# Performance work log

Measured on AMD Instinct MI355X. Metric: run time of the kernel, lower is better.

The kernel has to match this reference:

```python
import jax, jax.numpy as jnp
import numpy as np

N_DST = (50000, 25000, 12500)


def setup_inputs() -> dict:
    key = jax.random.key(0)
    ks = jax.random.split(key, 20)
    d_in, d_h, d_out = 256, 256, 128
    n_src = 100000
    inp = {}
    inp["x"] = jax.random.normal(ks[0], (n_src, d_in), dtype=jnp.float32)
    s = lambda k, sh, fan: jax.random.normal(k, sh, dtype=jnp.float32) / np.sqrt(fan)
    inp["Wn0"] = s(ks[1], (d_in, d_h), d_in)
    inp["Ws0"] = s(ks[2], (d_in, d_h), d_in)
    inp["b0"] = jnp.zeros((d_h,), jnp.float32)
    inp["Wn1"] = s(ks[3], (d_h, d_h), d_h)
    inp["Ws1"] = s(ks[4], (d_h, d_h), d_h)
    inp["b1"] = jnp.zeros((d_h,), jnp.float32)
    inp["Wn2"] = s(ks[5], (d_h, d_out), d_h)
    inp["Ws2"] = s(ks[6], (d_h, d_out), d_h)
    inp["b2"] = jnp.zeros((d_out,), jnp.float32)
    inp["src0"] = jax.random.randint(ks[7], (500000,), 0, n_src, dtype=jnp.int32)
    inp["dst0"] = jax.random.randint(ks[8], (500000,), 0, N_DST[0], dtype=jnp.int32)
    inp["src1"] = jax.random.randint(ks[9], (250000,), 0, N_DST[0], dtype=jnp.int32)
    inp["dst1"] = jax.random.randint(ks[10], (250000,), 0, N_DST[1], dtype=jnp.int32)
    inp["src2"] = jax.random.randint(ks[11], (125000,), 0, N_DST[1], dtype=jnp.int32)
    inp["dst2"] = jax.random.randint(ks[12], (125000,), 0, N_DST[2], dtype=jnp.int32)
    return inp


def _sage_conv(h_src, src, dst, n_dst, Wn, Ws, b):
    # mean aggregation over incoming neighbors, then linear + self linear
    msg = h_src[src]                                   # [E, d] gather
    agg = jax.ops.segment_sum(msg, dst, num_segments=n_dst)
    cnt = jax.ops.segment_sum(jnp.ones((src.shape[0], 1), h_src.dtype), dst,
                              num_segments=n_dst)
    mean = agg / jnp.maximum(cnt, 1.0)
    return mean @ Wn + h_src[:n_dst] @ Ws + b


def reference(x, Wn0, Ws0, b0, Wn1, Ws1, b1, Wn2, Ws2, b2,
              src0, dst0, src1, dst1, src2, dst2):
    h = _sage_conv(x, src0, dst0, N_DST[0], Wn0, Ws0, b0)
    h = jax.nn.relu(h)
    h = _sage_conv(h, src1, dst1, N_DST[1], Wn1, Ws1, b1)
    h = jax.nn.relu(h)
    h = _sage_conv(h, src2, dst2, N_DST[2], Wn2, Ws2, b2)
    return h
```

## Files before the change

kernel.cpp:

```cpp
#include <hip/hip_runtime.h>
#include <hip/hip_bf16.h>


typedef __attribute__((ext_vector_type(8))) short bf16x8;
typedef __attribute__((ext_vector_type(4))) float floatx4;

constexpr int M0 = 50000, M1 = 25000, M2 = 12500;
constexpr int NODE_OFF1 = 50000, NODE_OFF2 = 75000, M_TOT = 87500;
constexpr int NSRC = 100000;
constexpr int NPART = 8;
constexpr int CAP = 64;

__device__ inline unsigned short f2bf(float f) {
    union { float f; unsigned int u; } v{f};
    unsigned int u = v.u;
    return (unsigned short)((u + 0x7FFFu + ((u >> 16) & 1u)) >> 16);
}
__device__ inline float bf2f(unsigned short h) {
    union { unsigned int u; float f; } v{(unsigned int)h << 16};
    return v.f;
}

constexpr int CAST_B = 25000;
constexpr int PREP_B = 640;

__global__ __launch_bounds__(256) void front_kernel(
    const float* __restrict__ x, unsigned short* __restrict__ xb,
    const float* __restrict__ Wn0, const float* __restrict__ Ws0,
    const float* __restrict__ Wn1, const float* __restrict__ Ws1,
    const float* __restrict__ Wn2, const float* __restrict__ Ws2,
    unsigned short* __restrict__ Wt0, unsigned short* __restrict__ Wt1,
    unsigned short* __restrict__ Wt2,
    const int* __restrict__ src0, const int* __restrict__ dst0,
    const int* __restrict__ src1, const int* __restrict__ dst1,
    const int* __restrict__ src2, const int* __restrict__ dst2,
    int* __restrict__ wptr, int* __restrict__ bkt,
    int E0, int E1, int E2)
{
    const int blk = blockIdx.x;
    if (blk < CAST_B) {
        long i = (long)blk * 256 + threadIdx.x;
        float4 v = reinterpret_cast<const float4*>(x)[i];
        ushort4 o{f2bf(v.x), f2bf(v.y), f2bf(v.z), f2bf(v.w)};
        reinterpret_cast<ushort4*>(xb)[i] = o;
    } else if (blk < CAST_B + PREP_B) {
        int b = blk - CAST_B;
        const float* Wn; const float* Ws; unsigned short* Wt; int N; int base;
        if (b < 256)      { Wn = Wn0; Ws = Ws0; Wt = Wt0; N = 256; base = 0; }
        else if (b < 512) { Wn = Wn1; Ws = Ws1; Wt = Wt1; N = 256; base = 256; }
        else              { Wn = Wn2; Ws = Ws2; Wt = Wt2; N = 128; base = 512; }
        int idx = (b - base) * 256 + threadIdx.x;
        int n = idx >> 8, k = idx & 255;
        if (n >= N) return;
        Wt[(size_t)n * 512 + k]       = f2bf(Wn[(size_t)k * N + n]);
        Wt[(size_t)n * 512 + 256 + k] = f2bf(Ws[(size_t)k * N + n]);
    } else {
        const int b = blk - CAST_B - PREP_B;
        const int part = b & (NPART - 1);
        const int i = (b >> 3) * 256 + threadIdx.x;
        const int lo = (int)(((long)M_TOT * part) / NPART);
        const int hi = (int)(((long)M_TOT * (part + 1)) / NPART);
        int node, s;
        if (i < E0) {
            node = dst0[i]; s = src0[i];
        } else if (i < E0 + E1) {
            int j = i - E0; node = NODE_OFF1 + dst1[j]; s = src1[j];
        } else if (i < E0 + E1 + E2) {
            int j = i - E0 - E1; node = NODE_OFF2 + dst2[j]; s = src2[j];
        } else return;
        if (node >= lo && node < hi) {
            int p = atomicAdd(&wptr[node], 1);
            if (p < CAP) bkt[(size_t)node * CAP + p] = s;
        }
    }
}


__global__ __launch_bounds__(256) void aggregate_mean_bf16(
    const unsigned short* __restrict__ h, const int* __restrict__ wptr,
    const int* __restrict__ bkt, unsigned short* __restrict__ mean, int M)
{
    int gid = blockIdx.x * 256 + threadIdx.x;
    int node = gid >> 6;
    int lane = gid & 63;
    if (node >= M) return;
    int cnt = min(wptr[node], CAP);
    const int* lst = bkt + (size_t)node * CAP;
    float ax = 0.f, ay = 0.f, az = 0.f, aw = 0.f;
    int e = 0;
    for (; e + 8 <= cnt; e += 8) {
        int sidx = lst[e + (lane & 7)];
#pragma unroll
        for (int j = 0; j < 8; ++j) {
            int s = __shfl(sidx, j);
            ushort4 v = *(const ushort4*)(h + (size_t)s * 256 + lane * 4);
            ax += bf2f(v.x); ay += bf2f(v.y); az += bf2f(v.z); aw += bf2f(v.w);
        }
    }
    for (; e < cnt; ++e) {
        int s = lst[e];
        ushort4 v = *(const ushort4*)(h + (size_t)s * 256 + lane * 4);
        ax += bf2f(v.x); ay += bf2f(v.y); az += bf2f(v.z); aw += bf2f(v.w);
    }
    float invd = 1.0f / (float)max(cnt, 1);
    ushort4 o{f2bf(ax * invd), f2bf(ay * invd), f2bf(az * invd), f2bf(aw * invd)};
    *(ushort4*)(mean + (size_t)node * 256 + lane * 4) = o;
}


template <int RELU, int OUT_BF16>
__global__ __launch_bounds__(256) void sage_mfma(
    const unsigned short* __restrict__ A1,
    const unsigned short* __restrict__ A2,
    const unsigned short* __restrict__ Wt,
    const float* __restrict__ bias,
    void* __restrict__ out, int M, int N)
{
    constexpr int PK = 64 + 8;
    __shared__ unsigned short sA[128][PK];
    __shared__ unsigned short sB[128][PK];

    const int tid = threadIdx.x;
    const int bm = blockIdx.y * 128;
    const int bn = blockIdx.x * 128;
    const int wid = tid >> 6, lane = tid & 63;
    const int wm = (wid >> 1) * 64;
    const int wn = (wid & 1) * 64;
    const int quad = lane >> 4, l16 = lane & 15;

    const int sr = tid >> 1;
    const int sc = (tid & 1) * 32;

    floatx4 acc[4][4] = {};

    for (int k0 = 0; k0 < 512; k0 += 64) {
        const unsigned short* Ab = (k0 < 256) ? A1 : A2;
        const int ak = k0 & 255;
        const float4* ag = (const float4*)(Ab + (size_t)(bm + sr) * 256 + ak + sc);
        float4 a0 = ag[0], a1 = ag[1], a2 = ag[2], a3 = ag[3];
        const float4* bg = (const float4*)(Wt + (size_t)(bn + sr) * 512 + k0 + sc);
        float4 b0 = bg[0], b1 = bg[1], b2 = bg[2], b3 = bg[3];
        __syncthreads();
        *(float4*)&sA[sr][sc]      = a0;
        *(float4*)&sA[sr][sc + 8]  = a1;
        *(float4*)&sA[sr][sc + 16] = a2;
        *(float4*)&sA[sr][sc + 24] = a3;
        *(float4*)&sB[sr][sc]      = b0;
        *(float4*)&sB[sr][sc + 8]  = b1;
        *(float4*)&sB[sr][sc + 16] = b2;
        *(float4*)&sB[sr][sc + 24] = b3;
        __syncthreads();
#pragma unroll
        for (int ks = 0; ks < 64; ks += 32) {
            bf16x8 af[4], bfr[4];
#pragma unroll
            for (int i = 0; i < 4; ++i)
                af[i] = *(const bf16x8*)&sA[wm + i * 16 + l16][ks + quad * 8];
#pragma unroll
            for (int j = 0; j < 4; ++j)
                bfr[j] = *(const bf16x8*)&sB[wn + j * 16 + l16][ks + quad * 8];
#pragma unroll
            for (int i = 0; i < 4; ++i)
#pragma unroll
                for (int j = 0; j < 4; ++j)
                    acc[i][j] = __builtin_amdgcn_mfma_f32_16x16x32_bf16(
                        af[i], bfr[j], acc[i][j], 0, 0, 0);
        }
    }

#pragma unroll
    for (int j = 0; j < 4; ++j) {
        int col = bn + wn + j * 16 + l16;
        float bcol = bias[col];
#pragma unroll
        for (int i = 0; i < 4; ++i) {
#pragma unroll
            for (int r = 0; r < 4; ++r) {
                int row = bm + wm + i * 16 + quad * 4 + r;
                if (row < M) {
                    float v = acc[i][j][r] + bcol;
                    if (RELU) v = fmaxf(v, 0.0f);
                    if (OUT_BF16)
                        ((unsigned short*)out)[(size_t)row * N + col] = f2bf(v);
                    else
                        ((float*)out)[(size_t)row * N + col] = v;
                }
            }
        }
    }
}


extern "C" void kernel_launch(void* const* d_in, const int* in_sizes, int n_in,
                              void* d_out, int out_size, void* d_ws, size_t ws_size,
                              hipStream_t stream)
{
    const float* x   = (const float*)d_in[0];
    const float* Wn0 = (const float*)d_in[1];
    const float* Ws0 = (const float*)d_in[2];
    const float* b0  = (const float*)d_in[3];
    const float* Wn1 = (const float*)d_in[4];
    const float* Ws1 = (const float*)d_in[5];
    const float* b1  = (const float*)d_in[6];
    const float* Wn2 = (const float*)d_in[7];
    const float* Ws2 = (const float*)d_in[8];
    const float* b2  = (const float*)d_in[9];
    const int* src0 = (const int*)d_in[10];
    const int* dst0 = (const int*)d_in[11];
    const int* src1 = (const int*)d_in[12];
    const int* dst1 = (const int*)d_in[13];
    const int* src2 = (const int*)d_in[14];
    const int* dst2 = (const int*)d_in[15];
    const int E0 = in_sizes[10], E1 = in_sizes[12], E2 = in_sizes[14];
    const int E_tot = E0 + E1 + E2;

    unsigned short* xb   = (unsigned short*)d_ws;
    unsigned short* mean = xb   + (size_t)NSRC  * 256;
    unsigned short* h0   = mean + (size_t)50048 * 256;
    unsigned short* h1   = h0   + (size_t)50048 * 256;
    unsigned short* Wt0  = h1   + (size_t)25088 * 256;
    unsigned short* Wt1  = Wt0  + 256 * 512;
    unsigned short* Wt2  = Wt1  + 256 * 512;
    int* wptr   = (int*)(Wt2 + 128 * 512);
    int* bkt    = wptr + M_TOT;
    float* outp = (float*)d_out;

    hipMemsetAsync(wptr, 0, (size_t)M_TOT * sizeof(int), stream);

    const int sc_b = (E_tot + 255) / 256;
    front_kernel<<<dim3(CAST_B + PREP_B + NPART * sc_b), dim3(256), 0, stream>>>(
        x, xb, Wn0, Ws0, Wn1, Ws1, Wn2, Ws2, Wt0, Wt1, Wt2,
        src0, dst0, src1, dst1, src2, dst2, wptr, bkt, E0, E1, E2);

    auto run_layer = [&](const unsigned short* hin, int node_off, int M,
                         const unsigned short* Wt, const float* b,
                         void* hout, int N, bool relu, bool out_bf16) {
        aggregate_mean_bf16<<<dim3((M * 64 + 255) / 256), dim3(256), 0, stream>>>(
            hin, wptr + node_off, bkt + (size_t)node_off * CAP, mean, M);
        dim3 g(N / 128, (M + 127) / 128);
        if (out_bf16)
            sage_mfma<1, 1><<<g, dim3(256), 0, stream>>>(mean, hin, Wt, b, hout, M, N);
        else
            sage_mfma<0, 0><<<g, dim3(256), 0, stream>>>(mean, hin, Wt, b, hout, M, N);
    };

    run_layer(xb, 0,         M0, Wt0, b0, h0,   256, true,  true);
    run_layer(h0, NODE_OFF1, M1, Wt1, b1, h1,   256, true,  true);
    run_layer(h1, NODE_OFF2, M2, Wt2, b2, outp, 128, false, false);
}
```

Before: 392.8 us.

## Interleave cast and scatter blocks; aggregate two nodes per wavefront

The front kernel now interleaves its x-cast blocks with the edge-scatter blocks, so bandwidth-bound casting overlaps with atomic-heavy bucketing instead of running in separate phases, and the weight-prep blocks move to the end. The aggregation kernel now has each wavefront process two destination nodes at once: it loads the whole neighbor list with one coalesced read per node and issues the two nodes' gathers in the same loop, giving more memory-level parallelism. This risks divergence when the two nodes' degrees differ and halves the number of launched waves.

New measurement: 409.1 us. 4.1% more time.

```diff
diff --git a/kernel.cpp b/kernel.cpp
--- a/kernel.cpp
+++ b/kernel.cpp
@@ -35,29 +35,32 @@
     const int* __restrict__ src1, const int* __restrict__ dst1,
     const int* __restrict__ src2, const int* __restrict__ dst2,
     int* __restrict__ wptr, int* __restrict__ bkt,
-    int E0, int E1, int E2)
-{
-    const int blk = blockIdx.x;
-    if (blk < CAST_B) {
-        long i = (long)blk * 256 + threadIdx.x;
+    int E0, int E1, int E2, int SC_B)
+{
+    const int b = blockIdx.x;
+    const int minb = (CAST_B < SC_B) ? CAST_B : SC_B;
+    const int inter = 2 * minb;
+    int role, idx;
+    if (b < inter) {
+        role = b & 1;
+        idx = b >> 1;
+    } else {
+        int r = b - inter;
+        int scatRem = SC_B - minb;
+        int castRem = CAST_B - minb;
+        if (r < scatRem)                { role = 1; idx = minb + r; }
+        else if (r < scatRem + castRem) { role = 0; idx = minb + (r - scatRem); }
+        else                            { role = 2; idx = r - scatRem - castRem; }
+    }
+
+    if (role == 0) {
+        long i = (long)idx * 256 + threadIdx.x;
         float4 v = reinterpret_cast<const float4*>(x)[i];
         ushort4 o{f2bf(v.x), f2bf(v.y), f2bf(v.z), f2bf(v.w)};
         reinterpret_cast<ushort4*>(xb)[i] = o;
-    } else if (blk < CAST_B + PREP_B) {
-        int b = blk - CAST_B;
-        const float* Wn; const float* Ws; unsigned short* Wt; int N; int base;
-        if (b < 256)      { Wn = Wn0; Ws = Ws0; Wt = Wt0; N = 256; base = 0; }
-        else if (b < 512) { Wn = Wn1; Ws = Ws1; Wt = Wt1; N = 256; base = 256; }
-        else              { Wn = Wn2; Ws = Ws2; Wt = Wt2; N = 128; base = 512; }
-        int idx = (b - base) * 256 + threadIdx.x;
-        int n = idx >> 8, k = idx & 255;
-        if (n >= N) return;
-        Wt[(size_t)n * 512 + k]       = f2bf(Wn[(size_t)k * N + n]);
-        Wt[(size_t)n * 512 + 256 + k] = f2bf(Ws[(size_t)k * N + n]);
-    } else {
-        const int b = blk - CAST_B - PREP_B;
-        const int part = b & (NPART - 1);
-        const int i = (b >> 3) * 256 + threadIdx.x;
+    } else if (role == 1) {
+        const int part = idx & (NPART - 1);
+        const int i = (idx >> 3) * 256 + threadIdx.x;
         const int lo = (int)(((long)M_TOT * part) / NPART);
         const int hi = (int)(((long)M_TOT * (part + 1)) / NPART);
         int node, s;
@@ -72,6 +75,17 @@
             int p = atomicAdd(&wptr[node], 1);
             if (p < CAP) bkt[(size_t)node * CAP + p] = s;
         }
+    } else {
+        int bb = idx;
+        const float* Wn; const float* Ws; unsigned short* Wt; int N; int base;
+        if (bb < 256)      { Wn = Wn0; Ws = Ws0; Wt = Wt0; N = 256; base = 0; }
+        else if (bb < 512) { Wn = Wn1; Ws = Ws1; Wt = Wt1; N = 256; base = 256; }
+        else               { Wn = Wn2; Ws = Ws2; Wt = Wt2; N = 128; base = 512; }
+        int idx2 = (bb - base) * 256 + threadIdx.x;
+        int n = idx2 >> 8, k = idx2 & 255;
+        if (n >= N) return;
+        Wt[(size_t)n * 512 + k]       = f2bf(Wn[(size_t)k * N + n]);
+        Wt[(size_t)n * 512 + 256 + k] = f2bf(Ws[(size_t)k * N + n]);
     }
 }
 
@@ -81,30 +95,39 @@
     const int* __restrict__ bkt, unsigned short* __restrict__ mean, int M)
 {
     int gid = blockIdx.x * 256 + threadIdx.x;
-    int node = gid >> 6;
+    int w = gid >> 6;
     int lane = gid & 63;
-    if (node >= M) return;
-    int cnt = min(wptr[node], CAP);
-    const int* lst = bkt + (size_t)node * CAP;
-    float ax = 0.f, ay = 0.f, az = 0.f, aw = 0.f;
-    int e = 0;
-    for (; e + 8 <= cnt; e += 8) {
-        int sidx = lst[e + (lane & 7)];
-#pragma unroll
-        for (int j = 0; j < 8; ++j) {
-            int s = __shfl(sidx, j);
+    int half = (M + 1) >> 1;
+    if (w >= half) return;
+    int n0 = w, n1 = w + half;
+    bool has1 = (n1 < M);
+    int c0 = min(wptr[n0], CAP);
+    int c1 = has1 ? min(wptr[n1], CAP) : 0;
+    int sidx0 = bkt[(size_t)n0 * CAP + lane];
+    int sidx1 = has1 ? bkt[(size_t)n1 * CAP + lane] : 0;
+    float a0x = 0.f, a0y = 0.f, a0z = 0.f, a0w = 0.f;
+    float a1x = 0.f, a1y = 0.f, a1z = 0.f, a1w = 0.f;
+    int mx = max(c0, c1);
+    for (int j = 0; j < mx; ++j) {
+        if (j < c0) {
+            int s = __shfl(sidx0, j);
             ushort4 v = *(const ushort4*)(h + (size_t)s * 256 + lane * 4);
-            ax += bf2f(v.x); ay += bf2f(v.y); az += bf2f(v.z); aw += bf2f(v.w);
-        }
-    }
-    for (; e < cnt; ++e) {
-        int s = lst[e];
-        ushort4 v = *(const ushort4*)(h + (size_t)s * 256 + lane * 4);
-        ax += bf2f(v.x); ay += bf2f(v.y); az += bf2f(v.z); aw += bf2f(v.w);
-    }
-    float invd = 1.0f / (float)max(cnt, 1);
-    ushort4 o{f2bf(ax * invd), f2bf(ay * invd), f2bf(az * invd), f2bf(aw * invd)};
-    *(ushort4*)(mean + (size_t)node * 256 + lane * 4) = o;
+            a0x += bf2f(v.x); a0y += bf2f(v.y); a0z += bf2f(v.z); a0w += bf2f(v.w);
+        }
+        if (j < c1) {
+            int s = __shfl(sidx1, j);
+            ushort4 v = *(const ushort4*)(h + (size_t)s * 256 + lane * 4);
+            a1x += bf2f(v.x); a1y += bf2f(v.y); a1z += bf2f(v.z); a1w += bf2f(v.w);
+        }
+    }
+    float i0 = 1.0f / (float)max(c0, 1);
+    ushort4 o0{f2bf(a0x * i0), f2bf(a0y * i0), f2bf(a0z * i0), f2bf(a0w * i0)};
+    *(ushort4*)(mean + (size_t)n0 * 256 + lane * 4) = o0;
+    if (has1) {
+        float i1 = 1.0f / (float)max(c1, 1);
+        ushort4 o1{f2bf(a1x * i1), f2bf(a1y * i1), f2bf(a1z * i1), f2bf(a1w * i1)};
+        *(ushort4*)(mean + (size_t)n1 * 256 + lane * 4) = o1;
+    }
 }
 
 
@@ -228,14 +251,16 @@
     hipMemsetAsync(wptr, 0, (size_t)M_TOT * sizeof(int), stream);
 
     const int sc_b = (E_tot + 255) / 256;
-    front_kernel<<<dim3(CAST_B + PREP_B + NPART * sc_b), dim3(256), 0, stream>>>(
+    const int SC_B = NPART * sc_b;
+    front_kernel<<<dim3(CAST_B + PREP_B + SC_B), dim3(256), 0, stream>>>(
         x, xb, Wn0, Ws0, Wn1, Ws1, Wn2, Ws2, Wt0, Wt1, Wt2,
-        src0, dst0, src1, dst1, src2, dst2, wptr, bkt, E0, E1, E2);
+        src0, dst0, src1, dst1, src2, dst2, wptr, bkt, E0, E1, E2, SC_B);
 
     auto run_layer = [&](const unsigned short* hin, int node_off, int M,
                          const unsigned short* Wt, const float* b,
                          void* hout, int N, bool relu, bool out_bf16) {
-        aggregate_mean_bf16<<<dim3((M * 64 + 255) / 256), dim3(256), 0, stream>>>(
+        int halfw = (M + 1) >> 1;
+        aggregate_mean_bf16<<<dim3((halfw * 64 + 255) / 256), dim3(256), 0, stream>>>(
             hin, wptr + node_off, bkt + (size_t)node_off * CAP, mean, M);
         dim3 g(N / 128, (M + 127) / 128);
         if (out_bf16)
```

## Fuse all stages into one persistent cooperative kernel with grid syncs

Applied to the files above, without the earlier changes.

Replaces the memset plus seven separate launches with a single cooperative persistent kernel that loops over work units in grid-stride fashion and separates stages with grid.sync. The aim is to remove launch overhead and inter-kernel gaps. The aggregation now loads the whole bucket list with one coalesced read and picks indices with shuffles. The risk is that persistent blocks, capped at three per CU by launch bounds, underfill the wide cast and gather stages. Shared memory from the GEMM also limits occupancy in the memory-bound phases.

Measured after the change: 1.041 ms. 165% more time.

```diff
diff --git a/kernel.cpp b/kernel.cpp
--- a/kernel.cpp
+++ b/kernel.cpp
@@ -1,5 +1,8 @@
 #include <hip/hip_runtime.h>
 #include <hip/hip_bf16.h>
+#include <hip/hip_cooperative_groups.h>
+
+namespace cg = cooperative_groups;
 
 
 typedef __attribute__((ext_vector_type(8))) short bf16x8;
@@ -10,6 +13,20 @@
 constexpr int NSRC = 100000;
 constexpr int NPART = 8;
 constexpr int CAP = 64;
+constexpr int PK = 72;
+constexpr int CAST_B = 25000;
+constexpr int PREP_B = 640;
+
+struct SageArgs {
+    const float* x;
+    const float *Wn0, *Ws0, *Wn1, *Ws1, *Wn2, *Ws2;
+    const float *b0, *b1, *b2;
+    const int *src0, *dst0, *src1, *dst1, *src2, *dst2;
+    int E0, E1, E2, SC_B;
+    unsigned short *xb, *mean, *h0, *h1, *Wt0, *Wt1, *Wt2;
+    int *wptr, *bkt;
+    float* out;
+};
 
 __device__ inline unsigned short f2bf(float f) {
     union { float f; unsigned int u; } v{f};
@@ -21,173 +38,215 @@
     return v.f;
 }
 
-constexpr int CAST_B = 25000;
-constexpr int PREP_B = 640;
-
-__global__ __launch_bounds__(256) void front_kernel(
-    const float* __restrict__ x, unsigned short* __restrict__ xb,
-    const float* __restrict__ Wn0, const float* __restrict__ Ws0,
-    const float* __restrict__ Wn1, const float* __restrict__ Ws1,
-    const float* __restrict__ Wn2, const float* __restrict__ Ws2,
-    unsigned short* __restrict__ Wt0, unsigned short* __restrict__ Wt1,
-    unsigned short* __restrict__ Wt2,
-    const int* __restrict__ src0, const int* __restrict__ dst0,
-    const int* __restrict__ src1, const int* __restrict__ dst1,
-    const int* __restrict__ src2, const int* __restrict__ dst2,
-    int* __restrict__ wptr, int* __restrict__ bkt,
-    int E0, int E1, int E2)
-{
-    const int blk = blockIdx.x;
-    if (blk < CAST_B) {
-        long i = (long)blk * 256 + threadIdx.x;
-        float4 v = reinterpret_cast<const float4*>(x)[i];
-        ushort4 o{f2bf(v.x), f2bf(v.y), f2bf(v.z), f2bf(v.w)};
-        reinterpret_cast<ushort4*>(xb)[i] = o;
-    } else if (blk < CAST_B + PREP_B) {
-        int b = blk - CAST_B;
-        const float* Wn; const float* Ws; unsigned short* Wt; int N; int base;
-        if (b < 256)      { Wn = Wn0; Ws = Ws0; Wt = Wt0; N = 256; base = 0; }
-        else if (b < 512) { Wn = Wn1; Ws = Ws1; Wt = Wt1; N = 256; base = 256; }
-        else              { Wn = Wn2; Ws = Ws2; Wt = Wt2; N = 128; base = 512; }
-        int idx = (b - base) * 256 + threadIdx.x;
-        int n = idx >> 8, k = idx & 255;
-        if (n >= N) return;
-        Wt[(size_t)n * 512 + k]       = f2bf(Wn[(size_t)k * N + n]);
-        Wt[(size_t)n * 512 + 256 + k] = f2bf(Ws[(size_t)k * N + n]);
-    } else {
-        const int b = blk - CAST_B - PREP_B;
-        const int part = b & (NPART - 1);
-        const int i = (b >> 3) * 256 + threadIdx.x;
-        const int lo = (int)(((long)M_TOT * part) / NPART);
-        const int hi = (int)(((long)M_TOT * (part + 1)) / NPART);
-        int node, s;
-        if (i < E0) {
-            node = dst0[i]; s = src0[i];
-        } else if (i < E0 + E1) {
-            int j = i - E0; node = NODE_OFF1 + dst1[j]; s = src1[j];
-        } else if (i < E0 + E1 + E2) {
-            int j = i - E0 - E1; node = NODE_OFF2 + dst2[j]; s = src2[j];
-        } else return;
-        if (node >= lo && node < hi) {
-            int p = atomicAdd(&wptr[node], 1);
-            if (p < CAP) bkt[(size_t)node * CAP + p] = s;
+__device__ __forceinline__ void stage_zero(const SageArgs& a, int nb)
+{
+    for (int i = blockIdx.x * 256 + threadIdx.x; i < M_TOT; i += nb * 256)
+        a.wptr[i] = 0;
+}
+
+__device__ __forceinline__ void stage_front(const SageArgs& a, int nb)
+{
+    const int E0 = a.E0, E1 = a.E1, E2 = a.E2;
+    const int units = CAST_B + PREP_B + a.SC_B;
+    for (int u = blockIdx.x; u < units; u += nb) {
+        if (u < CAST_B) {
+            long i = (long)u * 256 + threadIdx.x;
+            float4 v = reinterpret_cast<const float4*>(a.x)[i];
+            ushort4 o{f2bf(v.x), f2bf(v.y), f2bf(v.z), f2bf(v.w)};
+            reinterpret_cast<ushort4*>(a.xb)[i] = o;
+        } else if (u < CAST_B + PREP_B) {
+            int b = u - CAST_B;
+            const float* Wn; const float* Ws; unsigned short* Wt; int N; int base;
+            if (b < 256)      { Wn = a.Wn0; Ws = a.Ws0; Wt = a.Wt0; N = 256; base = 0; }
+            else if (b < 512) { Wn = a.Wn1; Ws = a.Ws1; Wt = a.Wt1; N = 256; base = 256; }
+            else              { Wn = a.Wn2; Ws = a.Ws2; Wt = a.Wt2; N = 128; base = 512; }
+            int idx = (b - base) * 256 + threadIdx.x;
+            int n = idx >> 8, k = idx & 255;
+            if (n < N) {
+                Wt[(size_t)n * 512 + k]       = f2bf(Wn[(size_t)k * N + n]);
+                Wt[(size_t)n * 512 + 256 + k] = f2bf(Ws[(size_t)k * N + n]);
+            }
+        } else {
+            const int b = u - CAST_B - PREP_B;
+            const int part = b & (NPART - 1);
+            const int i = (b >> 3) * 256 + threadIdx.x;
+            const int lo = (int)(((long)M_TOT * part) / NPART);
+            const int hi = (int)(((long)M_TOT * (part + 1)) / NPART);
+            int node = -1, s = 0;
+            if (i < E0) {
+                node = a.dst0[i]; s = a.src0[i];
+            } else if (i < E0 + E1) {
+                int j = i - E0; node = NODE_OFF1 + a.dst1[j]; s = a.src1[j];
+            } else if (i < E0 + E1 + E2) {
+                int j = i - E0 - E1; node = NODE_OFF2 + a.dst2[j]; s = a.src2[j];
+            }
+            if (node >= lo && node < hi) {
+                int p = atomicAdd(&a.wptr[node], 1);
+                if (p < CAP) a.bkt[(size_t)node * CAP + p] = s;
+            }
         }
     }
 }
 
-
-__global__ __launch_bounds__(256) void aggregate_mean_bf16(
-    const unsigned short* __restrict__ h, const int* __restrict__ wptr,
-    const int* __restrict__ bkt, unsigned short* __restrict__ mean, int M)
-{
-    int gid = blockIdx.x * 256 + threadIdx.x;
-    int node = gid >> 6;
-    int lane = gid & 63;
-    if (node >= M) return;
-    int cnt = min(wptr[node], CAP);
-    const int* lst = bkt + (size_t)node * CAP;
-    float ax = 0.f, ay = 0.f, az = 0.f, aw = 0.f;
-    int e = 0;
-    for (; e + 8 <= cnt; e += 8) {
-        int sidx = lst[e + (lane & 7)];
-#pragma unroll
-        for (int j = 0; j < 8; ++j) {
-            int s = __shfl(sidx, j);
+__device__ __forceinline__ void stage_agg(
+    const unsigned short* __restrict__ h, const int* __restrict__ wp,
+    const int* __restrict__ bk, unsigned short* __restrict__ mean,
+    int M, int nb)
+{
+    const int lane = threadIdx.x & 63;
+    const int wid = threadIdx.x >> 6;
+    for (int node = blockIdx.x * 4 + wid; node < M; node += nb * 4) {
+        int cnt = min(wp[node], CAP);
+        int sidx = bk[(size_t)node * CAP + lane];
+        float ax = 0.f, ay = 0.f, az = 0.f, aw = 0.f;
+        int e = 0;
+        for (; e + 8 <= cnt; e += 8) {
+#pragma unroll
+            for (int j = 0; j < 8; ++j) {
+                int s = __shfl(sidx, e + j);
+                ushort4 v = *(const ushort4*)(h + (size_t)s * 256 + lane * 4);
+                ax += bf2f(v.x); ay += bf2f(v.y); az += bf2f(v.z); aw += bf2f(v.w);
+            }
+        }
+        for (; e < cnt; ++e) {
+            int s = __shfl(sidx, e);
             ushort4 v = *(const ushort4*)(h + (size_t)s * 256 + lane * 4);
             ax += bf2f(v.x); ay += bf2f(v.y); az += bf2f(v.z); aw += bf2f(v.w);
         }
+        float invd = 1.0f / (float)max(cnt, 1);
+        ushort4 o{f2bf(ax * invd), f2bf(ay * invd), f2bf(az * invd), f2bf(aw * invd)};
+        *(ushort4*)(mean + (size_t)node * 256 + lane * 4) = o;
     }
-    for (; e < cnt; ++e) {
-        int s = lst[e];
-        ushort4 v = *(const ushort4*)(h + (size_t)s * 256 + lane * 4);
-        ax += bf2f(v.x); ay += bf2f(v.y); az += bf2f(v.z); aw += bf2f(v.w);
-    }
-    float invd = 1.0f / (float)max(cnt, 1);
-    ushort4 o{f2bf(ax * invd), f2bf(ay * invd), f2bf(az * invd), f2bf(aw * invd)};
-    *(ushort4*)(mean + (size_t)node * 256 + lane * 4) = o;
-}
-
+}
 
 template <int RELU, int OUT_BF16>
-__global__ __launch_bounds__(256) void sage_mfma(
-    const unsigned short* __restrict__ A1,
-    const unsigned short* __restrict__ A2,
-    const unsigned short* __restrict__ Wt,
-    const float* __restrict__ bias,
-    void* __restrict__ out, int M, int N)
-{
-    constexpr int PK = 64 + 8;
-    __shared__ unsigned short sA[128][PK];
-    __shared__ unsigned short sB[128][PK];
-
+__device__ __forceinline__ void stage_gemm(
+    unsigned short (*sA)[PK], unsigned short (*sB)[PK],
+    const unsigned short* __restrict__ A1, const unsigned short* __restrict__ A2,
+    const unsigned short* __restrict__ Wt, const float* __restrict__ bias,
+    void* __restrict__ out, int M, int N, int nb)
+{
     const int tid = threadIdx.x;
-    const int bm = blockIdx.y * 128;
-    const int bn = blockIdx.x * 128;
+    const int tiles_m = (M + 127) >> 7;
+    const int tiles_n = N >> 7;
+    const int tiles = tiles_m * tiles_n;
     const int wid = tid >> 6, lane = tid & 63;
     const int wm = (wid >> 1) * 64;
     const int wn = (wid & 1) * 64;
     const int quad = lane >> 4, l16 = lane & 15;
-
     const int sr = tid >> 1;
     const int sc = (tid & 1) * 32;
 
-    floatx4 acc[4][4] = {};
-
-    for (int k0 = 0; k0 < 512; k0 += 64) {
-        const unsigned short* Ab = (k0 < 256) ? A1 : A2;
-        const int ak = k0 & 255;
-        const float4* ag = (const float4*)(Ab + (size_t)(bm + sr) * 256 + ak + sc);
-        float4 a0 = ag[0], a1 = ag[1], a2 = ag[2], a3 = ag[3];
-        const float4* bg = (const float4*)(Wt + (size_t)(bn + sr) * 512 + k0 + sc);
-        float4 b0 = bg[0], b1 = bg[1], b2 = bg[2], b3 = bg[3];
-        __syncthreads();
-        *(float4*)&sA[sr][sc]      = a0;
-        *(float4*)&sA[sr][sc + 8]  = a1;
-        *(float4*)&sA[sr][sc + 16] = a2;
-        *(float4*)&sA[sr][sc + 24] = a3;
-        *(float4*)&sB[sr][sc]      = b0;
-        *(float4*)&sB[sr][sc + 8]  = b1;
-        *(float4*)&sB[sr][sc + 16] = b2;
-        *(float4*)&sB[sr][sc + 24] = b3;
-        __syncthreads();
-#pragma unroll
-        for (int ks = 0; ks < 64; ks += 32) {
-            bf16x8 af[4], bfr[4];
-#pragma unroll
-            for (int i = 0; i < 4; ++i)
-                af[i] = *(const bf16x8*)&sA[wm + i * 16 + l16][ks + quad * 8];
-#pragma unroll
-            for (int j = 0; j < 4; ++j)
-                bfr[j] = *(const bf16x8*)&sB[wn + j * 16 + l16][ks + quad * 8];
-#pragma unroll
-            for (int i = 0; i < 4; ++i)
+    for (int t = blockIdx.x; t < tiles; t += nb) {
+        const int bm = (t / tiles_n) * 128;
+        const int bn = (t % tiles_n) * 128;
+        floatx4 acc[4][4] = {};
+
+        for (int k0 = 0; k0 < 512; k0 += 64) {
+            const unsigned short* Ab = (k0 < 256) ? A1 : A2;
+            const int ak = k0 & 255;
+            const float4* ag = (const float4*)(Ab + (size_t)(bm + sr) * 256 + ak + sc);
+            float4 a0 = ag[0], a1 = ag[1], a2 = ag[2], a3 = ag[3];
+            const float4* bg = (const float4*)(Wt + (size_t)(bn + sr) * 512 + k0 + sc);
+            float4 b0 = bg[0], b1 = bg[1], b2 = bg[2], b3 = bg[3];
+            __syncthreads();
+            *(float4*)&sA[sr][sc]      = a0;
+            *(float4*)&sA[sr][sc + 8]  = a1;
+            *(float4*)&sA[sr][sc + 16] = a2;
+            *(float4*)&sA[sr][sc + 24] = a3;
+            *(float4*)&sB[sr][sc]      = b0;
+            *(float4*)&sB[sr][sc + 8]  = b1;
+            *(float4*)&sB[sr][sc + 16] = b2;
+            *(float4*)&sB[sr][sc + 24] = b3;
+            __syncthreads();
+#pragma unroll
+            for (int ks = 0; ks < 64; ks += 32) {
+                bf16x8 af[4], bfr[4];
+#pragma unroll
+                for (int i = 0; i < 4; ++i)
+                    af[i] = *(const bf16x8*)&sA[wm + i * 16 + l16][ks + quad * 8];
 #pragma unroll
                 for (int j = 0; j < 4; ++j)
-                    acc[i][j] = __builtin_amdgcn_mfma_f32_16x16x32_bf16(
-                        af[i], bfr[j], acc[i][j], 0, 0, 0);
+                    bfr[j] = *(const bf16x8*)&sB[wn + j * 16 + l16][ks + quad * 8];
+#pragma unroll
+                for (int i = 0; i < 4; ++i)
+#pragma unroll
+                    for (int j = 0; j < 4; ++j)
+                        acc[i][j] = __builtin_amdgcn_mfma_f32_16x16x32_bf16(
+                            af[i], bfr[j], acc[i][j], 0, 0, 0);
+            }
+        }
+
+#pragma unroll
+        for (int j = 0; j < 4; ++j) {
+            int col = bn + wn + j * 16 + l16;
+            float bcol = bias[col];
+#pragma unroll
+            for (int i = 0; i < 4; ++i) {
+#pragma unroll
+                for (int r = 0; r < 4; ++r) {
+                    int row = bm + wm + i * 16 + quad * 4 + r;
+                    if (row < M) {
+                        float v = acc[i][j][r] + bcol;
+                        if (RELU) v = fmaxf(v, 0.0f);
+                        if (OUT_BF16)
+                            ((unsigned short*)out)[(size_t)row * N + col] = f2bf(v);
+                        else
+                            ((float*)out)[(size_t)row * N + col] = v;
+                    }
+                }
+            }
         }
     }
-
-#pragma unroll
-    for (int j = 0; j < 4; ++j) {
-        int col = bn + wn + j * 16 + l16;
-        float bcol = bias[col];
-#pragma unroll
-        for (int i = 0; i < 4; ++i) {
-#pragma unroll
-            for (int r = 0; r < 4; ++r) {
-                int row = bm + wm + i * 16 + quad * 4 + r;
-                if (row < M) {
-                    float v = acc[i][j][r] + bcol;
-                    if (RELU) v = fmaxf(v, 0.0f);
-                    if (OUT_BF16)
-                        ((unsigned short*)out)[(size_t)row * N + col] = f2bf(v);
-                    else
-                        ((float*)out)[(size_t)row * N + col] = v;
-                }
-            }
-        }
-    }
+}
+
+
+__global__ __launch_bounds__(256, 3) void sage_all(SageArgs a)
+{
+    __shared__ unsigned short sA[128][PK];
+    __shared__ unsigned short sB[128][PK];
+    cg::grid_group grid = cg::this_grid();
+    const int nb = gridDim.x;
+
+    stage_zero(a, nb);
+    __threadfence(); grid.sync();
+
+    stage_front(a, nb);
+    __threadfence(); grid.sync();
+
+    stage_agg(a.xb, a.wptr, a.bkt, a.mean, M0, nb);
+    __threadfence(); grid.sync();
+    stage_gemm<1, 1>(sA, sB, a.mean, a.xb, a.Wt0, a.b0, a.h0, M0, 256, nb);
+    __threadfence(); grid.sync();
+
+    stage_agg(a.h0, a.wptr + NODE_OFF1, a.bkt + (size_t)NODE_OFF1 * CAP, a.mean, M1, nb);
+    __threadfence(); grid.sync();
+    stage_gemm<1, 1>(sA, sB, a.mean, a.h0, a.Wt1, a.b1, a.h1, M1, 256, nb);
+    __threadfence(); grid.sync();
+
+    stage_agg(a.h1, a.wptr + NODE_OFF2, a.bkt + (size_t)NODE_OFF2 * CAP, a.mean, M2, nb);
+    __threadfence(); grid.sync();
+    stage_gemm<0, 0>(sA, sB, a.mean, a.h1, a.Wt2, a.b2, a.out, M2, 128, nb);
+}
+
+
+__global__ __launch_bounds__(256) void k_zero(SageArgs a) { stage_zero(a, gridDim.x); }
+__global__ __launch_bounds__(256) void k_front(SageArgs a) { stage_front(a, gridDim.x); }
+__global__ __launch_bounds__(256) void k_agg(SageArgs a, int layer)
+{
+    if (layer == 0)      stage_agg(a.xb, a.wptr, a.bkt, a.mean, M0, gridDim.x);
+    else if (layer == 1) stage_agg(a.h0, a.wptr + NODE_OFF1,
+                                   a.bkt + (size_t)NODE_OFF1 * CAP, a.mean, M1, gridDim.x);
+    else                 stage_agg(a.h1, a.wptr + NODE_OFF2,
+                                   a.bkt + (size_t)NODE_OFF2 * CAP, a.mean, M2, gridDim.x);
+}
+__global__ __launch_bounds__(256) void k_gemm(SageArgs a, int layer)
+{
+    __shared__ unsigned short sA[128][PK];
+    __shared__ unsigned short sB[128][PK];
+    if (layer == 0)      stage_gemm<1, 1>(sA, sB, a.mean, a.xb, a.Wt0, a.b0, a.h0, M0, 256, gridDim.x);
+    else if (layer == 1) stage_gemm<1, 1>(sA, sB, a.mean, a.h0, a.Wt1, a.b1, a.h1, M1, 256, gridDim.x);
+    else                 stage_gemm<0, 0>(sA, sB, a.mean, a.h1, a.Wt2, a.b2, a.out, M2, 128, gridDim.x);
 }
 
 
@@ -195,56 +254,51 @@
                               void* d_out, int out_size, void* d_ws, size_t ws_size,
                               hipStream_t stream)
 {
-    const float* x   = (const float*)d_in[0];
-    const float* Wn0 = (const float*)d_in[1];
-    const float* Ws0 = (const float*)d_in[2];
-    const float* b0  = (const float*)d_in[3];
-    const float* Wn1 = (const float*)d_in[4];
-    const float* Ws1 = (const float*)d_in[5];
-    const float* b1  = (const float*)d_in[6];
-    const float* Wn2 = (const float*)d_in[7];
-    const float* Ws2 = (const float*)d_in[8];
-    const float* b2  = (const float*)d_in[9];
-    const int* src0 = (const int*)d_in[10];
-    const int* dst0 = (const int*)d_in[11];
-    const int* src1 = (const int*)d_in[12];
-    const int* dst1 = (const int*)d_in[13];
-    const int* src2 = (const int*)d_in[14];
-    const int* dst2 = (const int*)d_in[15];
-    const int E0 = in_sizes[10], E1 = in_sizes[12], E2 = in_sizes[14];
-    const int E_tot = E0 + E1 + E2;
-
-    unsigned short* xb   = (unsigned short*)d_ws;
-    unsigned short* mean = xb   + (size_t)NSRC  * 256;
-    unsigned short* h0   = mean + (size_t)50048 * 256;
-    unsigned short* h1   = h0   + (size_t)50048 * 256;
-    unsigned short* Wt0  = h1   + (size_t)25088 * 256;
-    unsigned short* Wt1  = Wt0  + 256 * 512;
-    unsigned short* Wt2  = Wt1  + 256 * 512;
-    int* wptr   = (int*)(Wt2 + 128 * 512);
-    int* bkt    = wptr + M_TOT;
-    float* outp = (float*)d_out;
-
-    hipMemsetAsync(wptr, 0, (size_t)M_TOT * sizeof(int), stream);
-
-    const int sc_b = (E_tot + 255) / 256;
-    front_kernel<<<dim3(CAST_B + PREP_B + NPART * sc_b), dim3(256), 0, stream>>>(
-        x, xb, Wn0, Ws0, Wn1, Ws1, Wn2, Ws2, Wt0, Wt1, Wt2,
-        src0, dst0, src1, dst1, src2, dst2, wptr, bkt, E0, E1, E2);
-
-    auto run_layer = [&](const unsigned short* hin, int node_off, int M,
-                         const unsigned short* Wt, const float* b,
-                         void* hout, int N, bool relu, bool out_bf16) {
-        aggregate_mean_bf16<<<dim3((M * 64 + 255) / 256), dim3(256), 0, stream>>>(
-            hin, wptr + node_off, bkt + (size_t)node_off * CAP, mean, M);
-        dim3 g(N / 128, (M + 127) / 128);
-        if (out_bf16)
-            sage_mfma<1, 1><<<g, dim3(256), 0, stream>>>(mean, hin, Wt, b, hout, M, N);
-        else
-            sage_mfma<0, 0><<<g, dim3(256), 0, stream>>>(mean, hin, Wt, b, hout, M, N);
-    };
-
-    run_layer(xb, 0,         M0, Wt0, b0, h0,   256, true,  true);
-    run_layer(h0, NODE_OFF1, M1, Wt1, b1, h1,   256, true,  true);
-    run_layer(h1, NODE_OFF2, M2, Wt2, b2, outp, 128, false, false);
-}
+    SageArgs a;
+    a.x   = (const float*)d_in[0];
+    a.Wn0 = (const float*)d_in[1];  a.Ws0 = (const float*)d_in[2];
+    a.b0  = (const float*)d_in[3];
+    a.Wn1 = (const float*)d_in[4];  a.Ws1 = (const float*)d_in[5];
+    a.b1  = (const float*)d_in[6];
+    a.Wn2 = (const float*)d_in[7];  a.Ws2 = (const float*)d_in[8];
+    a.b2  = (const float*)d_in[9];
+    a.src0 = (const int*)d_in[10];  a.dst0 = (const int*)d_in[11];
+    a.src1 = (const int*)d_in[12];  a.dst1 = (const int*)d_in[13];
+    a.src2 = (const int*)d_in[14];  a.dst2 = (const int*)d_in[15];
+    a.E0 = in_sizes[10]; a.E1 = in_sizes[12]; a.E2 = in_sizes[14];
+    const int E_tot = a.E0 + a.E1 + a.E2;
+    a.SC_B = NPART * ((E_tot + 255) / 256);
+
+    a.xb   = (unsigned short*)d_ws;
+    a.mean = a.xb   + (size_t)NSRC  * 256;
+    a.h0   = a.mean + (size_t)50048 * 256;
+    a.h1   = a.h0   + (size_t)50048 * 256;
+    a.Wt0  = a.h1   + (size_t)25088 * 256;
+    a.Wt1  = a.Wt0  + 256 * 512;
+    a.Wt2  = a.Wt1  + 256 * 512;
+    a.wptr = (int*)(a.Wt2 + 128 * 512);
+    a.bkt  = a.wptr + M_TOT;
+    a.out  = (float*)d_out;
+
+    int maxb = 0;
+    hipError_t oe = hipOccupancyMaxActiveBlocksPerMultiprocessor(
+        &maxb, (const void*)sage_all, 256, 0);
+    int grid = (oe == hipSuccess && maxb > 0) ? maxb * 256 : 256;
+    if (grid > 768) grid = 768;
+
+    void* kargs[] = { (void*)&a };
+    hipError_t err = hipLaunchCooperativeKernel(
+        (const void*)sage_all, dim3(grid), dim3(256), kargs, 0, stream);
+
+    if (err != hipSuccess) {
+        k_zero<<<dim3(88), dim3(256), 0, stream>>>(a);
+        k_front<<<dim3(CAST_B + PREP_B + a.SC_B), dim3(256), 0, stream>>>(a);
+        for (int l = 0; l < 3; ++l) {
+            int M = (l == 0) ? M0 : (l == 1) ? M1 : M2;
+            int N = (l == 2) ? 128 : 256;
+            k_agg<<<dim3((M + 3) / 4), dim3(256), 0, stream>>>(a, l);
+            int tiles = ((M + 127) / 128) * (N / 128);
+            k_gemm<<<dim3(tiles), dim3(256), 0, stream>>>(a, l);
+        }
+    }
+}
```
